# Kernel optimization log

Measured on AMD Instinct MI355X. Metric: run time of the kernel, lower is better.

The kernel has to match this reference:

```python
import jax, jax.numpy as jnp
import numpy as np

P, T, D, H = 128, 2048, 128, 64   # parts, seq_len, in_channels, hidden_gru
OUT = 24                           # out_channels(1) * out_steps(24)

def setup_inputs() -> dict:
    key = jax.random.key(0)
    ks = jax.random.split(key, 13)
    s = 0.05
    return {
        "z":    jax.random.normal(ks[0], (P, T, D), jnp.float32),
        # per-part GRU params, torch gate order (r, z, n) stacked along dim 0 of 3H
        "w_ih": jax.random.normal(ks[1], (P, 3 * H, D), jnp.float32) * s,
        "w_hh": jax.random.normal(ks[2], (P, 3 * H, H), jnp.float32) * s,
        "b_ih": jax.random.normal(ks[3], (P, 3 * H), jnp.float32) * s,
        "b_hh": jax.random.normal(ks[4], (P, 3 * H), jnp.float32) * s,
        # per-part MLP: 64 -> 128 -> 64 -> 32 -> 24 (weights stored [out, in] like torch)
        "w1": jax.random.normal(ks[5], (P, 128, H), jnp.float32) * s,
        "b1": jax.random.normal(ks[6], (P, 128), jnp.float32) * s,
        "w2": jax.random.normal(ks[7], (P, 64, 128), jnp.float32) * s,
        "b2": jax.random.normal(ks[8], (P, 64), jnp.float32) * s,
        "w3": jax.random.normal(ks[9], (P, 32, 64), jnp.float32) * s,
        "b3": jax.random.normal(ks[10], (P, 32), jnp.float32) * s,
        "w4": jax.random.normal(ks[11], (P, OUT, 32), jnp.float32) * s,
        "b4": jax.random.normal(ks[12], (P, OUT), jnp.float32) * s,
    }

def _gru_all_parts(z, w_ih, w_hh, b_ih, b_hh):
    # z: [P,T,D] -> hidden sequence [P,T,H]; all parts batched, scan over time.
    x_proj = jnp.einsum('ptd,pgd->tpg', z, w_ih) + b_ih  # [T,P,3H]
    h0 = jnp.zeros((z.shape[0], w_hh.shape[-1]), z.dtype)

    def step(h, xp):                           # h: [P,H], xp: [P,3H]
        hp = jnp.einsum('ph,pgh->pg', h, w_hh) + b_hh
        xr, xz, xn = jnp.split(xp, 3, axis=-1)
        hr, hz, hn = jnp.split(hp, 3, axis=-1)
        r = jax.nn.sigmoid(xr + hr)
        u = jax.nn.sigmoid(xz + hz)
        n = jnp.tanh(xn + r * hn)
        h_new = (1.0 - u) * n + u * h
        return h_new, h_new

    _, hs = jax.lax.scan(step, h0, x_proj)     # [T,P,H]
    return jnp.transpose(hs, (1, 0, 2))        # [P,T,H]

def reference(z, w_ih, w_hh, b_ih, b_hh, w1, b1, w2, b2, w3, b3, w4, b4):
    hs = _gru_all_parts(z, w_ih, w_hh, b_ih, b_hh)                      # [P,T,H]
    a = jax.nn.relu(jnp.einsum('pth,poh->pto', hs, w1) + b1[:, None, :])
    a = jax.nn.relu(jnp.einsum('pth,poh->pto', a, w2) + b2[:, None, :])
    a = jax.nn.relu(jnp.einsum('pth,poh->pto', a, w3) + b3[:, None, :])
    out = jnp.einsum('pth,poh->pto', a, w4) + b4[:, None, :]            # [P,T,OUT]
    return out  # out_channels == 1, so no final reshape branch
```

## Files before the change

kernel.cpp:

```cpp
#include <hip/hip_runtime.h>

#define P_ 128
#define T_ 2048
#define D_ 128
#define H_ 64
#define G_ 192
#define OUT_ 24

typedef float v2f __attribute__((ext_vector_type(2)));

__device__ __forceinline__ float rcpf_(float x){ return __builtin_amdgcn_rcpf(x); }
__device__ __forceinline__ float sigmoidf_(float x){ return rcpf_(1.0f + __expf(-x)); }
__device__ __forceinline__ float tanhf_(float x){
  float e = __expf(2.0f*x);
  return 1.0f - 2.0f*rcpf_(e + 1.0f);
}

__global__ __launch_bounds__(256) void xproj_kernel(
    const float* __restrict__ z, const float* __restrict__ w_ih,
    const float* __restrict__ b_ih, float* __restrict__ xp,
    int t0, int tcLen)
{
  __shared__ float zl[64*132];
  const int p = blockIdx.y;
  const int tBase = blockIdx.x*64;
  const int tid = threadIdx.x;
  const float* zg = z + ((size_t)p*T_ + (size_t)(t0 + tBase))*D_;
  #pragma unroll
  for (int i=0;i<8;i++){
    int idx = tid + i*256;
    int r = idx >> 5, c = idx & 31;
    *(float4*)(zl + r*132 + c*4) = *(const float4*)(zg + (size_t)r*D_ + c*4);
  }
  __syncthreads();

  const int tg = tid & 15, ng = tid >> 4;
  const int n0 = ng*12, tr = tg*4;
  const float* wg = w_ih + (size_t)p*G_*D_;
  float acc[4][12];
  #pragma unroll
  for (int j=0;j<12;j++){
    float b = b_ih[p*G_ + n0 + j];
    #pragma unroll
    for (int i=0;i<4;i++) acc[i][j] = b;
  }
  #pragma unroll 4
  for (int k=0;k<D_;k+=4){
    float4 x4[4];
    #pragma unroll
    for (int i=0;i<4;i++) x4[i] = *(const float4*)(zl + (tr+i)*132 + k);
    #pragma unroll
    for (int j=0;j<12;j++){
      float4 w4 = *(const float4*)(wg + (size_t)(n0+j)*D_ + k);
      #pragma unroll
      for (int i=0;i<4;i++)
        acc[i][j] = fmaf(x4[i].x,w4.x, fmaf(x4[i].y,w4.y, fmaf(x4[i].z,w4.z, fmaf(x4[i].w,w4.w, acc[i][j]))));
    }
  }
  float* orow = xp + ((size_t)p*tcLen + tBase)*G_;
  #pragma unroll
  for (int i=0;i<4;i++){
    #pragma unroll
    for (int j3=0;j3<3;j3++){
      float4 v = make_float4(acc[i][j3*4+0],acc[i][j3*4+1],acc[i][j3*4+2],acc[i][j3*4+3]);
      *(float4*)(orow + (size_t)(tr+i)*G_ + n0 + j3*4) = v;
    }
  }
}

__global__ __launch_bounds__(192, 1) void gru_kernel(
    const float* __restrict__ xp, const float* __restrict__ w_hh,
    const float* __restrict__ b_hh, float* __restrict__ hs,
    float* __restrict__ hstate, int t0, int tcLen)
{
  __shared__ __align__(16) float hbc[3][64];
  __shared__ float gx[2][3][64];
  const int p = blockIdx.x;
  const int tid = threadIdx.x;
  const int w = tid >> 6;
  const int l = tid & 63;

  v2f wg2[32];
  {
    const float* Wg = w_hh + ((size_t)p*G_ + 64*w + l)*H_;
    #pragma unroll
    for (int i=0;i<16;i++){
      float4 a = *(const float4*)(Wg + 4*i);
      wg2[2*i]   = v2f{a.x, a.y};
      wg2[2*i+1] = v2f{a.z, a.w};
    }
  }
  const float bg = b_hh[p*G_ + 64*w + l];

  float h = 0.0f;
  if (t0 != 0) h = hstate[p*H_ + l];
  hbc[w][l] = h;

  const float* xrow = xp + (size_t)p*tcLen*G_;
  float xg_n = xrow[64*w + l];
  float xn_n = xrow[128 + l];
  float* hsrow = hs + ((size_t)p*T_ + (size_t)t0)*H_;

  for (int tl=0; tl<tcLen; ++tl){
    float xg = xg_n, xn = xn_n;
    int tn = (tl+1 < tcLen) ? tl+1 : tl;
    const float* xnrow = xrow + (size_t)tn*G_;
    xg_n = xnrow[64*w + l];
    xn_n = xnrow[128 + l];

    float4 h4[16];
    #pragma unroll
    for (int j=0;j<16;j++) h4[j] = *(const float4*)(&hbc[w][4*j]);
    __builtin_amdgcn_sched_barrier(0);

    v2f acc = v2f{bg, 0.0f};
    #pragma unroll
    for (int j=0;j<16;j++){
      v2f h2a = v2f{h4[j].x, h4[j].y};
      v2f h2b = v2f{h4[j].z, h4[j].w};
      acc = __builtin_elementwise_fma(wg2[2*j],   h2a, acc);
      acc = __builtin_elementwise_fma(wg2[2*j+1], h2b, acc);
    }
    float dot = acc.x + acc.y;

    float gval = (w < 2) ? sigmoidf_(xg + dot) : dot;
    gx[tl&1][w][l] = gval;
    asm volatile("s_waitcnt lgkmcnt(0)" ::: "memory");
    __builtin_amdgcn_s_barrier();
    asm volatile("" ::: "memory");
    float rv  = gx[tl&1][0][l];
    float uv  = gx[tl&1][1][l];
    float hnv = gx[tl&1][2][l];

    float n = tanhf_(xn + rv*hnv);
    h = fmaf(uv, h - n, n);
    hbc[w][l] = h;
    if (w == 0) hsrow[(size_t)tl*H_ + l] = h;
  }
  if (w == 0) hstate[p*H_ + l] = h;
}

template<int K, int N, int NPT, bool RELU, bool TOGLOBAL>
__device__ __forceinline__ void layer_(
    const float* __restrict__ Xl, const float* __restrict__ Wg,
    const float* __restrict__ bg, float* Yl, float* outg, int tid)
{
  constexpr int NG = N / NPT;
  constexpr int XS = K + 4;
  constexpr int YS = N + 4;
  const int tg = tid & 15, ng = tid >> 4;
  if (ng < NG){
    const int tr = tg*4, n0 = ng*NPT;
    float acc[4][NPT];
    #pragma unroll
    for (int j=0;j<NPT;j++){
      float b = bg[n0+j];
      #pragma unroll
      for (int i=0;i<4;i++) acc[i][j] = b;
    }
    #pragma unroll 4
    for (int k=0;k<K;k+=4){
      float4 x4[4];
      #pragma unroll
      for (int i=0;i<4;i++) x4[i] = *(const float4*)(Xl + (tr+i)*XS + k);
      #pragma unroll
      for (int j=0;j<NPT;j++){
        float4 w4 = *(const float4*)(Wg + (size_t)(n0+j)*K + k);
        #pragma unroll
        for (int i=0;i<4;i++)
          acc[i][j] = fmaf(x4[i].x,w4.x, fmaf(x4[i].y,w4.y, fmaf(x4[i].z,w4.z, fmaf(x4[i].w,w4.w, acc[i][j]))));
      }
    }
    #pragma unroll
    for (int i=0;i<4;i++){
      #pragma unroll
      for (int j=0;j<NPT;j++){
        float v = acc[i][j];
        if (RELU) v = fmaxf(v, 0.0f);
        if (TOGLOBAL) outg[(size_t)(tr+i)*OUT_ + n0 + j] = v;
        else          Yl[(tr+i)*YS + n0 + j] = v;
      }
    }
  }
}

__global__ __launch_bounds__(256) void mlp_kernel(
    const float* __restrict__ hs,
    const float* __restrict__ w1, const float* __restrict__ b1,
    const float* __restrict__ w2, const float* __restrict__ b2,
    const float* __restrict__ w3, const float* __restrict__ b3,
    const float* __restrict__ w4, const float* __restrict__ b4,
    float* __restrict__ out)
{
  __shared__ float bufA[64*68];
  __shared__ float bufB[64*132];
  const int p = blockIdx.y;
  const int t0 = blockIdx.x*64;
  const int tid = threadIdx.x;

  const float* hg = hs + ((size_t)p*T_ + (size_t)t0)*H_;
  #pragma unroll
  for (int i=0;i<4;i++){
    int idx = tid + i*256;
    int r = idx >> 4, c = idx & 15;
    *(float4*)(bufA + r*68 + c*4) = *(const float4*)(hg + (size_t)r*H_ + c*4);
  }
  __syncthreads();
  layer_<64,128,8,true,false>(bufA, w1 + (size_t)p*128*64, b1 + p*128, bufB, nullptr, tid);
  __syncthreads();
  layer_<128,64,4,true,false>(bufB, w2 + (size_t)p*64*128, b2 + p*64, bufA, nullptr, tid);
  __syncthreads();
  layer_<64,32,2,true,false>(bufA, w3 + (size_t)p*32*64, b3 + p*32, bufB, nullptr, tid);
  __syncthreads();
  float* og = out + ((size_t)p*T_ + (size_t)t0)*OUT_;
  layer_<32,24,2,false,true>(bufB, w4 + (size_t)p*24*32, b4 + p*24, nullptr, og, tid);
}

extern "C" void kernel_launch(void* const* d_in, const int* in_sizes, int n_in,
                              void* d_out, int out_size, void* d_ws, size_t ws_size,
                              hipStream_t stream)
{
  const float* z    = (const float*)d_in[0];
  const float* w_ih = (const float*)d_in[1];
  const float* w_hh = (const float*)d_in[2];
  const float* b_ih = (const float*)d_in[3];
  const float* b_hh = (const float*)d_in[4];
  const float* w1 = (const float*)d_in[5];
  const float* b1 = (const float*)d_in[6];
  const float* w2 = (const float*)d_in[7];
  const float* b2 = (const float*)d_in[8];
  const float* w3 = (const float*)d_in[9];
  const float* b3 = (const float*)d_in[10];
  const float* w4 = (const float*)d_in[11];
  const float* b4 = (const float*)d_in[12];
  float* out = (float*)d_out;

  const size_t hsBytes = (size_t)P_*T_*H_*sizeof(float);
  const size_t stBytes = (size_t)P_*H_*sizeof(float);
  int tc = 64;
  for (int cand = T_; cand >= 64; cand >>= 1){
    size_t need = (size_t)P_*cand*G_*sizeof(float) + hsBytes + stBytes;
    if (need <= ws_size){ tc = cand; break; }
  }
  float* xp     = (float*)d_ws;
  float* hsbuf  = (float*)((char*)d_ws + (size_t)P_*tc*G_*sizeof(float));
  float* hstate = hsbuf + (size_t)P_*T_*H_;

  for (int t0 = 0; t0 < T_; t0 += tc){
    xproj_kernel<<<dim3(tc/64, P_), 256, 0, stream>>>(z, w_ih, b_ih, xp, t0, tc);
    gru_kernel<<<dim3(P_), 192, 0, stream>>>(xp, w_hh, b_hh, hsbuf, hstate, t0, tc);
  }
  mlp_kernel<<<dim3(T_/64, P_), 256, 0, stream>>>(hsbuf, w1,b1,w2,b2,w3,b3,w4,b4, out);
}
```

Baseline: 1.505 ms.

## Split GRU recurrent dot product across two waves per gate

The GRU block now runs six waves instead of three: each gate's 64-wide hidden dot product is split into two 32-element halves held by separate waves, and the partial sums are combined after the barrier. Sigmoid and tanh are applied by every wave after the reduction. The x-projection prefetch now runs two timesteps ahead, using a two-step unrolled loop. The aim is to shorten the serial per-step latency of the recurrence, at the cost of more threads, more shared-memory reads and redundant activation math.

```diff
diff --git a/kernel.cpp b/kernel.cpp
--- a/kernel.cpp
+++ b/kernel.cpp
@@ -68,74 +68,89 @@
   }
 }
 
-__global__ __launch_bounds__(192, 1) void gru_kernel(
+__global__ __launch_bounds__(384, 1) void gru_kernel(
     const float* __restrict__ xp, const float* __restrict__ w_hh,
     const float* __restrict__ b_hh, float* __restrict__ hs,
     float* __restrict__ hstate, int t0, int tcLen)
 {
-  __shared__ __align__(16) float hbc[3][64];
-  __shared__ float gx[2][3][64];
-  const int p = blockIdx.x;
+  __shared__ __align__(16) float hbc[6][64];
+  __shared__ float gxp[2][6][64];
+  const int p   = blockIdx.x;
   const int tid = threadIdx.x;
-  const int w = tid >> 6;
-  const int l = tid & 63;
-
-  v2f wg2[32];
+  const int w   = tid >> 6;
+  const int g   = w >> 1;
+  const int hf  = w & 1;
+  const int l   = tid & 63;
+
+  v2f wg2[16];
   {
-    const float* Wg = w_hh + ((size_t)p*G_ + 64*w + l)*H_;
-    #pragma unroll
-    for (int i=0;i<16;i++){
+    const float* Wg = w_hh + ((size_t)p*G_ + 64*g + l)*H_ + 32*hf;
+    #pragma unroll
+    for (int i=0;i<8;i++){
       float4 a = *(const float4*)(Wg + 4*i);
       wg2[2*i]   = v2f{a.x, a.y};
       wg2[2*i+1] = v2f{a.z, a.w};
     }
   }
-  const float bg = b_hh[p*G_ + 64*w + l];
+  const float br = b_hh[p*G_ + l];
+  const float bz = b_hh[p*G_ + 64 + l];
+  const float bn = b_hh[p*G_ + 128 + l];
 
   float h = 0.0f;
   if (t0 != 0) h = hstate[p*H_ + l];
   hbc[w][l] = h;
 
   const float* xrow = xp + (size_t)p*tcLen*G_;
-  float xg_n = xrow[64*w + l];
-  float xn_n = xrow[128 + l];
   float* hsrow = hs + ((size_t)p*T_ + (size_t)t0)*H_;
 
-  for (int tl=0; tl<tcLen; ++tl){
-    float xg = xg_n, xn = xn_n;
-    int tn = (tl+1 < tcLen) ? tl+1 : tl;
-    const float* xnrow = xrow + (size_t)tn*G_;
-    xg_n = xnrow[64*w + l];
-    xn_n = xnrow[128 + l];
-
-    float4 h4[16];
-    #pragma unroll
-    for (int j=0;j<16;j++) h4[j] = *(const float4*)(&hbc[w][4*j]);
+  float xrA = xrow[l], xzA = xrow[64+l], xnA = xrow[128+l];
+  const float* x1 = xrow + G_;
+  float xrB = x1[l], xzB = x1[64+l], xnB = x1[128+l];
+
+  auto step = [&](float& xr, float& xz, float& xn, int tl){
+    const int b = tl & 1;
+    float4 h4[8];
+    #pragma unroll
+    for (int j=0;j<8;j++) h4[j] = *(const float4*)(&hbc[w][32*hf + 4*j]);
     __builtin_amdgcn_sched_barrier(0);
 
-    v2f acc = v2f{bg, 0.0f};
-    #pragma unroll
-    for (int j=0;j<16;j++){
-      v2f h2a = v2f{h4[j].x, h4[j].y};
-      v2f h2b = v2f{h4[j].z, h4[j].w};
-      acc = __builtin_elementwise_fma(wg2[2*j],   h2a, acc);
-      acc = __builtin_elementwise_fma(wg2[2*j+1], h2b, acc);
-    }
-    float dot = acc.x + acc.y;
-
-    float gval = (w < 2) ? sigmoidf_(xg + dot) : dot;
-    gx[tl&1][w][l] = gval;
+    v2f a0 = v2f{0.0f, 0.0f}, a1 = v2f{0.0f, 0.0f};
+    #pragma unroll
+    for (int j=0;j<4;j++){
+      v2f hA = v2f{h4[2*j].x,   h4[2*j].y};
+      v2f hB = v2f{h4[2*j].z,   h4[2*j].w};
+      v2f hC = v2f{h4[2*j+1].x, h4[2*j+1].y};
+      v2f hD = v2f{h4[2*j+1].z, h4[2*j+1].w};
+      a0 = __builtin_elementwise_fma(wg2[4*j],   hA, a0);
+      a1 = __builtin_elementwise_fma(wg2[4*j+1], hB, a1);
+      a0 = __builtin_elementwise_fma(wg2[4*j+2], hC, a0);
+      a1 = __builtin_elementwise_fma(wg2[4*j+3], hD, a1);
+    }
+    v2f as = a0 + a1;
+    gxp[b][w][l] = as.x + as.y;
+
     asm volatile("s_waitcnt lgkmcnt(0)" ::: "memory");
     __builtin_amdgcn_s_barrier();
     asm volatile("" ::: "memory");
-    float rv  = gx[tl&1][0][l];
-    float uv  = gx[tl&1][1][l];
-    float hnv = gx[tl&1][2][l];
-
-    float n = tanhf_(xn + rv*hnv);
-    h = fmaf(uv, h - n, n);
+
+    float dr = gxp[b][0][l] + gxp[b][1][l] + br;
+    float du = gxp[b][2][l] + gxp[b][3][l] + bz;
+    float dn = gxp[b][4][l] + gxp[b][5][l] + bn;
+    float r = sigmoidf_(xr + dr);
+    float u = sigmoidf_(xz + du);
+    float n = tanhf_(fmaf(r, dn, xn));
+    h = fmaf(u, h - n, n);
     hbc[w][l] = h;
     if (w == 0) hsrow[(size_t)tl*H_ + l] = h;
+
+    int tn = tl + 2; if (tn >= tcLen) tn = tcLen - 1;
+    const float* xf = xrow + (size_t)tn*G_;
+    xr = xf[l]; xz = xf[64+l]; xn = xf[128+l];
+  };
+
+  for (int tl = 0; tl < tcLen; tl += 2){
+    step(xrA, xzA, xnA, tl);
+    step(xrB, xzB, xnB, tl+1);
   }
   if (w == 0) hstate[p*H_ + l] = h;
 }
@@ -248,7 +263,7 @@
 
   for (int t0 = 0; t0 < T_; t0 += tc){
     xproj_kernel<<<dim3(tc/64, P_), 256, 0, stream>>>(z, w_ih, b_ih, xp, t0, tc);
-    gru_kernel<<<dim3(P_), 192, 0, stream>>>(xp, w_hh, b_hh, hsbuf, hstate, t0, tc);
+    gru_kernel<<<dim3(P_), 384, 0, stream>>>(xp, w_hh, b_hh, hsbuf, hstate, t0, tc);
   }
   mlp_kernel<<<dim3(T_/64, P_), 256, 0, stream>>>(hsbuf, w1,b1,w2,b2,w3,b3,w4,b4, out);
 }
```

After: 1.338 ms. 11.1% less time.
